# Kernel optimization log

Hardware: AMD Instinct MI355X
Metric: run time of the kernel (lower is better)

Reference implementation:

```python
import jax, jax.numpy as jnp
import numpy as np

MAX_SEQ_LEN = 1000

def _ln(x, g, b, eps=1e-5):
    m = jnp.mean(x, -1, keepdims=True)
    v = jnp.var(x, -1, keepdims=True)
    return (x - m) * jax.lax.rsqrt(v + eps) * g + b

def _conv1d(x, k, b):
    # x [B,T,Cin], k [K,Cin,Cout], 'SAME' padding (odd kernel)
    return jax.lax.conv_general_dilated(x, k, (1,), 'SAME', dimension_numbers=('NWC', 'WIO', 'NWC')) + b

def _dwconv(x, w):
    # lightweight conv: softmax-normalized depthwise kernel, w [C,K]
    k = jnp.transpose(jax.nn.softmax(w, axis=1))[:, None, :]  # [K,1,C]
    return jax.lax.conv_general_dilated(x, k, (1,), 'SAME', dimension_numbers=('NWC', 'WIO', 'NWC'), feature_group_count=x.shape[-1])

def _conv2d(x, k, b):
    # x [B,H,W,Cin], k [kh,kw,Cin,Cout]
    return jax.lax.conv_general_dilated(x, k, (1, 1), 'SAME', dimension_numbers=('NHWC', 'HWIO', 'NHWC')) + b

def _lconv(x, mask, ln_g, ln_b, glu_w, glu_b, dw, out_w, out_b):
    # LConvBlock: LN -> GLU projection -> depthwise lightweight conv -> out proj -> residual, masked
    res = x
    h = _ln(x, ln_g, ln_b)
    h = h @ glu_w + glu_b
    a, g = jnp.split(h, 2, axis=-1)
    h = a * jax.nn.sigmoid(g)
    h = jnp.where(mask[..., None], 0.0, h)
    h = _dwconv(h, dw)
    h = h @ out_w + out_b
    h = h + res
    return jnp.where(mask[..., None], 0.0, h)

def _forward(content_embedding, speaker_embedding_B, rhythm_B, scaled_duration_outputs,
             in_w, in_b,
             lc0_ln_g, lc0_ln_b, lc0_glu_w, lc0_glu_b, lc0_dw, lc0_out_w, lc0_out_b,
             lc1_ln_g, lc1_ln_b, lc1_glu_w, lc1_glu_b, lc1_dw, lc1_out_w, lc1_out_b,
             p1_w, p1_b, p2_k, p2_b,
             cw_k, cw_b, cw_ln_g, cw_ln_b,
             mkb1_k, mkb1_b, mkb2_k, mkb2_b,
             lw_w, lw_b, ln_g, ln_b, text_mask):
    B, S, _ = content_embedding.shape
    spk = jnp.broadcast_to(speaker_embedding_B[:, None, :], (B, S, speaker_embedding_B.shape[-1]))
    x = jnp.concatenate([content_embedding, spk], -1) @ in_w + in_b
    # duration predictor
    V = _lconv(x, text_mask, lc0_ln_g, lc0_ln_b, lc0_glu_w, lc0_glu_b, lc0_dw, lc0_out_w, lc0_out_b)
    V = _lconv(V, text_mask, lc1_ln_g, lc1_ln_b, lc1_glu_w, lc1_glu_b, lc1_dw, lc1_out_w, lc1_out_b)
    D = jax.nn.softplus(V @ p1_w + p1_b)[..., 0]
    D = jnp.where(text_mask, 0.0, D)
    T = _conv1d(V, p2_k, p2_b)  # [B,S,upsampled_dim]
    # learnable upsampling
    pred_phoneme_len = scaled_duration_outputs.sum(-1)
    alpha_B = jax.lax.stop_gradient(pred_phoneme_len / rhythm_B) / D.sum(-1)
    sD = alpha_B[:, None] * D
    sV = alpha_B[:, None, None] * V
    sT = alpha_B[:, None, None] * T
    mel_len = jnp.clip(jnp.round(sD.sum(-1)).astype(jnp.int32), 1, MAX_SEQ_LEN)
    mel_mask = jnp.arange(MAX_SEQ_LEN)[None, :] >= mel_len[:, None]  # True = pad
    attn_mask = mel_mask[:, :, None] & text_mask[:, None, :]  # bmm(mel_mask, src_mask^T).bool()
    e_k = jnp.cumsum(sD, axis=1)
    s_k = e_k - sD
    t = jnp.arange(1, MAX_SEQ_LEN + 1, dtype=sD.dtype)[None, :, None]
    Sm = jnp.where(attn_mask, 0.0, t - s_k[:, None, :])
    Em = jnp.where(attn_mask, 0.0, e_k[:, None, :] - t)
    # conv_w block: conv1d -> relu -> LN
    Cv = _ln(jax.nn.relu(_conv1d(sV, cw_k, cw_b)), cw_ln_g, cw_ln_b)  # [B,S,CW]
    feat = jnp.concatenate([Sm[..., None], Em[..., None],
                            jnp.broadcast_to(Cv[:, None, :, :], (B, MAX_SEQ_LEN, S, Cv.shape[-1]))], -1)
    h = jax.nn.silu(_conv2d(feat, mkb1_k, mkb1_b))
    h = jax.nn.silu(_conv2d(h, mkb2_k, mkb2_b))
    Wsc = (h @ lw_w + lw_b)[..., 0]  # [B,mel,S]
    Wsc = jnp.where(attn_mask | text_mask[:, None, :], -jnp.inf, Wsc)
    Wmat = jax.nn.softmax(Wsc, axis=2)
    up = jnp.matmul(Wmat, sT)
    up = _ln(up, ln_g, ln_b)
    up = jnp.where(mel_mask[..., None], 0.0, up)
    return up, Wmat, alpha_B, mel_len, mel_mask

def setup_inputs() -> dict:
    key = jax.random.key(0)
    ks = iter(jax.random.split(key, 64))
    B, S, DC, DS, H, CW, MKB, K = 8, 256, 192, 64, 256, 16, 16, 3
    def w(shape, scale=0.02):
        return jax.random.normal(next(ks), shape, jnp.float32) * scale
    inp = {}
    inp['content_embedding'] = jax.random.normal(next(ks), (B, S, DC), jnp.float32)
    inp['speaker_embedding_B'] = jax.random.normal(next(ks), (B, DS), jnp.float32)
    inp['rhythm_B'] = 0.15 + 0.1 * jax.random.uniform(next(ks), (B,), jnp.float32)
    inp['scaled_duration_outputs'] = jax.random.uniform(next(ks), (B, S), jnp.float32)
    lens = jax.random.randint(next(ks), (B,), 200, S + 1)
    inp['text_mask'] = jnp.arange(S)[None, :] >= lens[:, None]
    inp['in_w'] = w((DC + DS, H)); inp['in_b'] = jnp.zeros((H,), jnp.float32)
    for i in range(2):
        inp[f'lc{i}_ln_g'] = jnp.ones((H,), jnp.float32); inp[f'lc{i}_ln_b'] = jnp.zeros((H,), jnp.float32)
        inp[f'lc{i}_glu_w'] = w((H, 2 * H)); inp[f'lc{i}_glu_b'] = jnp.zeros((2 * H,), jnp.float32)
        inp[f'lc{i}_dw'] = w((H, K), 1.0)
        inp[f'lc{i}_out_w'] = w((H, H)); inp[f'lc{i}_out_b'] = jnp.zeros((H,), jnp.float32)
    inp['p1_w'] = w((H, 1)); inp['p1_b'] = jnp.zeros((1,), jnp.float32)
    inp['p2_k'] = w((K, H, H)); inp['p2_b'] = jnp.zeros((H,), jnp.float32)
    inp['cw_k'] = w((K, H, CW)); inp['cw_b'] = jnp.zeros((CW,), jnp.float32)
    inp['cw_ln_g'] = jnp.ones((CW,), jnp.float32); inp['cw_ln_b'] = jnp.zeros((CW,), jnp.float32)
    inp['mkb1_k'] = w((K, K, CW + 2, MKB)); inp['mkb1_b'] = jnp.zeros((MKB,), jnp.float32)
    inp['mkb2_k'] = w((K, K, MKB, MKB)); inp['mkb2_b'] = jnp.zeros((MKB,), jnp.float32)
    inp['lw_w'] = w((MKB, 1)); inp['lw_b'] = jnp.zeros((1,), jnp.float32)
    inp['ln_g'] = jnp.ones((H,), jnp.float32); inp['ln_b'] = jnp.zeros((H,), jnp.float32)
    return inp

def reference(content_embedding, speaker_embedding_B, rhythm_B, scaled_duration_outputs,
              text_mask,
              in_w, in_b,
              lc0_ln_g, lc0_ln_b, lc0_glu_w, lc0_glu_b, lc0_dw, lc0_out_w, lc0_out_b,
              lc1_ln_g, lc1_ln_b, lc1_glu_w, lc1_glu_b, lc1_dw, lc1_out_w, lc1_out_b,
              p1_w, p1_b, p2_k, p2_b,
              cw_k, cw_b, cw_ln_g, cw_ln_b,
              mkb1_k, mkb1_b, mkb2_k, mkb2_b,
              lw_w, lw_b, ln_g, ln_b):
    return _forward(content_embedding, speaker_embedding_B, rhythm_B, scaled_duration_outputs,
                    in_w, in_b,
                    lc0_ln_g, lc0_ln_b, lc0_glu_w, lc0_glu_b, lc0_dw, lc0_out_w, lc0_out_b,
                    lc1_ln_g, lc1_ln_b, lc1_glu_w, lc1_glu_b, lc1_dw, lc1_out_w, lc1_out_b,
                    p1_w, p1_b, p2_k, p2_b,
                    cw_k, cw_b, cw_ln_g, cw_ln_b,
                    mkb1_k, mkb1_b, mkb2_k, mkb2_b,
                    lw_w, lw_b, ln_g, ln_b, text_mask)
```

## Files before the change

### kernel.cpp

```cpp
#include <hip/hip_runtime.h>
#include <math.h>

#define SS 256
#define HH 256
#define MLEN 1000
#define CWW 16
#define NOC 16
#define RB 24

typedef __attribute__((ext_vector_type(8))) short bfrag;
typedef __attribute__((ext_vector_type(4))) float ffrag;

#define WS_V2     1048576u
#define WS_STT    1835008u
#define WS_WB     2097152u
#define WS_CCV    2424832u
#define WS_SSV    2457600u
#define WS_CCI    2490368u
#define WS_SSI    2523136u
#define WS_CP     2555904u
#define WS_CV     2654208u
#define WS_EK     2686976u
#define WS_SK     2689024u
#define WS_ALPHA  2691072u
#define WS_MELI   2691080u
#define WS_TMASK  2691088u

#define PK_IN     0u
#define PK_GLU0   65536u
#define PK_GLU1   196608u
#define PK_OUT0   327680u
#define PK_OUT1   393216u
#define PK_P2     458752u

#define OUT_UP    0u
#define OUT_W     2048000u
#define OUT_ALPHA 4096000u
#define OUT_MLEN  4096008u
#define OUT_MMASK 4096016u

__device__ __forceinline__ unsigned bf16rne(float x){
  unsigned u=__float_as_uint(x);
  u += 0x7fffu + ((u>>16)&1u);
  return u;
}
__device__ __forceinline__ unsigned short bf16h(float x){ return (unsigned short)(bf16rne(x)>>16); }
__device__ __forceinline__ float bf2f(unsigned short u){ return __uint_as_float(((unsigned)u)<<16); }
__device__ __forceinline__ unsigned frag_idx(int k,int n,int KT){
  return (unsigned)(((((n>>4)*KT+(k>>5))*64 + ((k>>3)&3)*16 + (n&15))<<3) + (k&7));
}

__global__ __launch_bounds__(256) void k_prepmask(const void* __restrict__ traw,
    const float* __restrict__ in_w,
    const float* __restrict__ g0, const float* __restrict__ g1,
    const float* __restrict__ o0, const float* __restrict__ o1,
    const float* __restrict__ p2k, float* __restrict__ ws){
  int tid=threadIdx.x;
  if(blockIdx.x==256){
    __shared__ int s_fu, s_ff, s_nz;
    const unsigned char* mb=(const unsigned char*)traw;
    const unsigned int*  mw=(const unsigned int*)traw;
    if(tid==0){s_fu=0;s_ff=0;s_nz=0;}
    __syncthreads();
    int fu=0,ff=0,nz=0;
    for(int w=tid;w<512;w+=256){
      unsigned int v=mw[w];
      if(v){ nz=1; if(v==0x3F800000u) ff=1; else if(v&0xFFFFFF00u) fu=1; }
    }
    if(fu) atomicOr(&s_fu,1);
    if(ff) atomicOr(&s_ff,1);
    if(nz) atomicOr(&s_nz,1);
    __syncthreads();
    int words = (s_ff || (!s_fu && s_nz));
    for(int i=tid;i<2048;i+=256){
      unsigned int v = words ? mw[i] : (unsigned int)mb[i];
      ws[WS_TMASK+i] = v ? 1.0f : 0.0f;
    }
    return;
  }
  unsigned short* wb=(unsigned short*)(ws+WS_WB);
  int gid=blockIdx.x*256+tid, stride=65536;
  for(int i=gid;i<65536;i+=stride){ int k=i>>8,n=i&255; wb[PK_IN  +frag_idx(k,n,8)]=bf16h(in_w[i]); }
  for(int i=gid;i<131072;i+=stride){ int k=i>>9,n=i&511; wb[PK_GLU0+frag_idx(k,n,8)]=bf16h(g0[i]); }
  for(int i=gid;i<131072;i+=stride){ int k=i>>9,n=i&511; wb[PK_GLU1+frag_idx(k,n,8)]=bf16h(g1[i]); }
  for(int i=gid;i<65536;i+=stride){ int k=i>>8,n=i&255; wb[PK_OUT0+frag_idx(k,n,8)]=bf16h(o0[i]); }
  for(int i=gid;i<65536;i+=stride){ int k=i>>8,n=i&255; wb[PK_OUT1+frag_idx(k,n,8)]=bf16h(o1[i]); }
  for(int i=gid;i<196608;i+=stride){ int k3=i>>16,r=i&65535,k=r>>8,n=r&255;
    wb[PK_P2+(unsigned)k3*65536u+frag_idx(k,n,8)]=bf16h(p2k[i]); }
}

__global__ __launch_bounds__(256) void k_front(
    const float* __restrict__ ce, const float* __restrict__ spk,
    const unsigned short* __restrict__ wb, const float* __restrict__ in_b,
    const float* __restrict__ g0b, const float* __restrict__ ln0g, const float* __restrict__ ln0b,
    const float* __restrict__ dw0, const float* __restrict__ o0b,
    const float* __restrict__ g1b, const float* __restrict__ ln1g, const float* __restrict__ ln1b,
    const float* __restrict__ dw1, const float* __restrict__ o1b,
    const float* __restrict__ tmask, float* __restrict__ V2){
  __shared__ unsigned short Abf[16][264];
  __shared__ unsigned short Hb[8][264];
  __shared__ float Xf[8][264];
  __shared__ float Vf[8][264];
  __shared__ float dws[2][3][256];
  __shared__ float tmL[8];
  int b=blockIdx.x>>6, tile=blockIdx.x&63, s0=tile*4, tid=threadIdx.x;
  int w=tid>>6, lane=tid&63, lq=lane>>4, lm=lane&15;
  {
    float d0=dw0[tid*3],d1=dw0[tid*3+1],d2=dw0[tid*3+2];
    float mx=fmaxf(d0,fmaxf(d1,d2));
    float e0=__expf(d0-mx),e1=__expf(d1-mx),e2=__expf(d2-mx);
    float inv=1.0f/(e0+e1+e2);
    dws[0][0][tid]=e0*inv; dws[0][1][tid]=e1*inv; dws[0][2][tid]=e2*inv;
    d0=dw1[tid*3];d1=dw1[tid*3+1];d2=dw1[tid*3+2];
    mx=fmaxf(d0,fmaxf(d1,d2));
    e0=__expf(d0-mx);e1=__expf(d1-mx);e2=__expf(d2-mx);
    inv=1.0f/(e0+e1+e2);
    dws[1][0][tid]=e0*inv; dws[1][1][tid]=e1*inv; dws[1][2][tid]=e2*inv;
  }
  if(tid<8){
    int sI=s0-2+tid;
    tmL[tid]=(sI>=0&&sI<256)? tmask[b*256+sI] : 1.0f;
  }
  for(int it=0;it<8;it++){
    float v=0.f;
    int sI=s0-2+it;
    if(sI>=0 && sI<256){
      int m=b*256+sI;
      v=(tid<192)? ce[m*192+tid] : spk[b*64+tid-192];
    }
    Abf[it][tid]=bf16h(v);
  }
  for(int it=8;it<16;it++) Abf[it][tid]=0;
  __syncthreads();
  {
    ffrag acc[4];
    #pragma unroll
    for(int j=0;j<4;j++){acc[j][0]=0;acc[j][1]=0;acc[j][2]=0;acc[j][3]=0;}
    #pragma unroll
    for(int kt=0;kt<8;kt++){
      bfrag af=*(const bfrag*)&Abf[lm][kt*32+lq*8];
      #pragma unroll
      for(int j=0;j<4;j++){
        int nt=w*4+j;
        bfrag bf=*(const bfrag*)(wb+PK_IN+((((unsigned)(nt*8+kt))*64u+(unsigned)lane)<<3));
        acc[j]=__builtin_amdgcn_mfma_f32_16x16x32_bf16(af,bf,acc[j],0,0,0);
      }
    }
    #pragma unroll
    for(int j=0;j<4;j++){
      int n=w*64+j*16+lm;
      float bn=in_b[n];
      #pragma unroll
      for(int reg=0;reg<4;reg++){
        int row=lq*4+reg;
        if(row<8) Xf[row][n]=acc[j][reg]+bn;
      }
    }
  }
  __syncthreads();
  {
    int r=tid>>4, seg=tid&15;
    if(r<8){
      float s=0.f,q=0.f;
      #pragma unroll
      for(int j4=0;j4<4;j4++){
        float4 v=*(const float4*)&Xf[r][seg*16+j4*4];
        s+=v.x+v.y+v.z+v.w; q+=v.x*v.x+v.y*v.y+v.z*v.z+v.w*v.w;
      }
      s+=__shfl_xor(s,1); q+=__shfl_xor(q,1);
      s+=__shfl_xor(s,2); q+=__shfl_xor(q,2);
      s+=__shfl_xor(s,4); q+=__shfl_xor(q,4);
      s+=__shfl_xor(s,8); q+=__shfl_xor(q,8);
      float mean=s*(1.0f/256.0f), rstd=rsqrtf(q*(1.0f/256.0f)-mean*mean+1e-5f);
      #pragma unroll
      for(int j4=0;j4<4;j4++){
        int c=seg*16+j4*4;
        float4 v=*(const float4*)&Xf[r][c];
        unsigned short q0=bf16h((v.x-mean)*rstd*ln0g[c+0]+ln0b[c+0]);
        unsigned short q1=bf16h((v.y-mean)*rstd*ln0g[c+1]+ln0b[c+1]);
        unsigned short q2=bf16h((v.z-mean)*rstd*ln0g[c+2]+ln0b[c+2]);
        unsigned short q3=bf16h((v.w-mean)*rstd*ln0g[c+3]+ln0b[c+3]);
        *(uint2*)&Abf[r][c]=make_uint2((unsigned)q0|((unsigned)q1<<16),(unsigned)q2|((unsigned)q3<<16));
      }
    }
  }
  __syncthreads();
  {
    ffrag aa[4],ag[4];
    #pragma unroll
    for(int j=0;j<4;j++){aa[j][0]=0;aa[j][1]=0;aa[j][2]=0;aa[j][3]=0;
                         ag[j][0]=0;ag[j][1]=0;ag[j][2]=0;ag[j][3]=0;}
    #pragma unroll
    for(int kt=0;kt<8;kt++){
      bfrag af=*(const bfrag*)&Abf[lm][kt*32+lq*8];
      #pragma unroll
      for(int j=0;j<4;j++){
        int nta=w*4+j, ntg=nta+16;
        bfrag bfa=*(const bfrag*)(wb+PK_GLU0+((((unsigned)(nta*8+kt))*64u+(unsigned)lane)<<3));
        bfrag bfg=*(const bfrag*)(wb+PK_GLU0+((((unsigned)(ntg*8+kt))*64u+(unsigned)lane)<<3));
        aa[j]=__builtin_amdgcn_mfma_f32_16x16x32_bf16(af,bfa,aa[j],0,0,0);
        ag[j]=__builtin_amdgcn_mfma_f32_16x16x32_bf16(af,bfg,ag[j],0,0,0);
      }
    }
    __syncthreads();
    #pragma unroll
    for(int j=0;j<4;j++){
      int n=w*64+j*16+lm;
      float ba=g0b[n], bg=g0b[n+256];
      #pragma unroll
      for(int reg=0;reg<4;reg++){
        int row=lq*4+reg;
        if(row<8){
          float a=aa[j][reg]+ba, g=ag[j][reg]+bg;
          float hv=a*(1.0f/(1.0f+__expf(-g)));
          if(tmL[row]!=0.0f) hv=0.0f;
          Hb[row][n]=bf16h(hv);
        }
      }
    }
  }
  __syncthreads();
  {
    float w0=dws[0][0][tid],w1=dws[0][1][tid],w2=dws[0][2][tid];
    for(int r=0;r<6;r++){
      float a=w0*bf2f(Hb[r][tid])+w1*bf2f(Hb[r+1][tid])+w2*bf2f(Hb[r+2][tid]);
      Abf[r][tid]=bf16h(a);
    }
    Abf[6][tid]=0; Abf[7][tid]=0;
  }
  __syncthreads();
  {
    ffrag acc[4];
    #pragma unroll
    for(int j=0;j<4;j++){acc[j][0]=0;acc[j][1]=0;acc[j][2]=0;acc[j][3]=0;}
    #pragma unroll
    for(int kt=0;kt<8;kt++){
      bfrag af=*(const bfrag*)&Abf[lm][kt*32+lq*8];
      #pragma unroll
      for(int j=0;j<4;j++){
        int nt=w*4+j;
        bfrag bf=*(const bfrag*)(wb+PK_OUT0+((((unsigned)(nt*8+kt))*64u+(unsigned)lane)<<3));
        acc[j]=__builtin_amdgcn_mfma_f32_16x16x32_bf16(af,bf,acc[j],0,0,0);
      }
    }
    #pragma unroll
    for(int j=0;j<4;j++){
      int n=w*64+j*16+lm;
      float bn=o0b[n];
      #pragma unroll
      for(int reg=0;reg<4;reg++){
        int row=lq*4+reg;
        if(row<6){
          float v=(tmL[row+1]==0.0f)? acc[j][reg]+bn+Xf[row+1][n] : 0.0f;
          Vf[row][n]=v;
        }
      }
    }
  }
  __syncthreads();
  {
    int r=tid>>4, seg=tid&15;
    if(r<6){
      float s=0.f,q=0.f;
      #pragma unroll
      for(int j4=0;j4<4;j4++){
        float4 v=*(const float4*)&Vf[r][seg*16+j4*4];
        s+=v.x+v.y+v.z+v.w; q+=v.x*v.x+v.y*v.y+v.z*v.z+v.w*v.w;
      }
      s+=__shfl_xor(s,1); q+=__shfl_xor(q,1);
      s+=__shfl_xor(s,2); q+=__shfl_xor(q,2);
      s+=__shfl_xor(s,4); q+=__shfl_xor(q,4);
      s+=__shfl_xor(s,8); q+=__shfl_xor(q,8);
      float mean=s*(1.0f/256.0f), rstd=rsqrtf(q*(1.0f/256.0f)-mean*mean+1e-5f);
      #pragma unroll
      for(int j4=0;j4<4;j4++){
        int c=seg*16+j4*4;
        float4 v=*(const float4*)&Vf[r][c];
        unsigned short q0=bf16h((v.x-mean)*rstd*ln1g[c+0]+ln1b[c+0]);
        unsigned short q1=bf16h((v.y-mean)*rstd*ln1g[c+1]+ln1b[c+1]);
        unsigned short q2=bf16h((v.z-mean)*rstd*ln1g[c+2]+ln1b[c+2]);
        unsigned short q3=bf16h((v.w-mean)*rstd*ln1g[c+3]+ln1b[c+3]);
        *(uint2*)&Abf[r][c]=make_uint2((unsigned)q0|((unsigned)q1<<16),(unsigned)q2|((unsigned)q3<<16));
      }
    }
  }
  __syncthreads();
  {
    ffrag aa[4],ag[4];
    #pragma unroll
    for(int j=0;j<4;j++){aa[j][0]=0;aa[j][1]=0;aa[j][2]=0;aa[j][3]=0;
                         ag[j][0]=0;ag[j][1]=0;ag[j][2]=0;ag[j][3]=0;}
    #pragma unroll
    for(int kt=0;kt<8;kt++){
      bfrag af=*(const bfrag*)&Abf[lm][kt*32+lq*8];
      #pragma unroll
      for(int j=0;j<4;j++){
        int nta=w*4+j, ntg=nta+16;
        bfrag bfa=*(const bfrag*)(wb+PK_GLU1+((((unsigned)(nta*8+kt))*64u+(unsigned)lane)<<3));
        bfrag bfg=*(const bfrag*)(wb+PK_GLU1+((((unsigned)(ntg*8+kt))*64u+(unsigned)lane)<<3));
        aa[j]=__builtin_amdgcn_mfma_f32_16x16x32_bf16(af,bfa,aa[j],0,0,0);
        ag[j]=__builtin_amdgcn_mfma_f32_16x16x32_bf16(af,bfg,ag[j],0,0,0);
      }
    }
    __syncthreads();
    #pragma unroll
    for(int j=0;j<4;j++){
      int n=w*64+j*16+lm;
      float ba=g1b[n], bg=g1b[n+256];
      #pragma unroll
      for(int reg=0;reg<4;reg++){
        int row=lq*4+reg;
        if(row<6){
          float a=aa[j][reg]+ba, g=ag[j][reg]+bg;
          float hv=a*(1.0f/(1.0f+__expf(-g)));
          if(tmL[row+1]!=0.0f) hv=0.0f;
          Hb[row][n]=bf16h(hv);
        }
      }
    }
  }
  __syncthreads();
  {
    float w0=dws[1][0][tid],w1=dws[1][1][tid],w2=dws[1][2][tid];
    for(int r=0;r<4;r++){
      float a=w0*bf2f(Hb[r][tid])+w1*bf2f(Hb[r+1][tid])+w2*bf2f(Hb[r+2][tid]);
      Abf[r][tid]=bf16h(a);
    }
    Abf[4][tid]=0; Abf[5][tid]=0;
  }
  __syncthreads();
  {
    ffrag acc[4];
    #pragma unroll
    for(int j=0;j<4;j++){acc[j][0]=0;acc[j][1]=0;acc[j][2]=0;acc[j][3]=0;}
    #pragma unroll
    for(int kt=0;kt<8;kt++){
      bfrag af=*(const bfrag*)&Abf[lm][kt*32+lq*8];
      #pragma unroll
      for(int j=0;j<4;j++){
        int nt=w*4+j;
        bfrag bf=*(const bfrag*)(wb+PK_OUT1+((((unsigned)(nt*8+kt))*64u+(unsigned)lane)<<3));
        acc[j]=__builtin_amdgcn_mfma_f32_16x16x32_bf16(af,bf,acc[j],0,0,0);
      }
    }
    #pragma unroll
    for(int j=0;j<4;j++){
      int n=w*64+j*16+lm;
      float bn=o1b[n];
      #pragma unroll
      for(int reg=0;reg<4;reg++){
        int row=lq*4+reg;
        if(row<4){
          float v=(tmL[row+2]!=0.0f)? 0.0f : acc[j][reg]+bn+Vf[row+1][n];
          V2[(unsigned)(b*256+s0+row)*256u+n]=v;
        }
      }
    }
  }
}

__global__ __launch_bounds__(256) void k_postdur(const float* __restrict__ V2,
    const unsigned short* __restrict__ wbp2, const float* __restrict__ p2b,
    const float* __restrict__ cwk,
    const float* __restrict__ p1w, const float* __restrict__ p1b,
    const float* __restrict__ sdo, const float* __restrict__ rhythm,
    float* __restrict__ ws, float* __restrict__ outp){
  int bx=blockIdx.x, tid=threadIdx.x;
  if(bx<256){
    __shared__ unsigned short Abf[18][264];
    int m0=(bx>>1)*16, nh=bx&1, b=m0>>8, s0=m0&255;
    for(int it=0;it<18;it++){
      int sI=s0-1+it;
      float v=(sI>=0&&sI<256)? V2[(unsigned)(b*256+sI)*256u+tid] : 0.0f;
      Abf[it][tid]=bf16h(v);
    }
    __syncthreads();
    int w=tid>>6, lane=tid&63, lq=lane>>4, lm=lane&15;
    ffrag acc[2];
    #pragma unroll
    for(int tt=0;tt<2;tt++){ acc[tt][0]=0;acc[tt][1]=0;acc[tt][2]=0;acc[tt][3]=0; }
    for(int k3=0;k3<3;k3++){
      const unsigned short* wb3=wbp2+(unsigned)k3*65536u;
      #pragma unroll
      for(int kt=0;kt<8;kt++){
        bfrag af=*(const bfrag*)&Abf[lm+k3][kt*32+lq*8];
        #pragma unroll
        for(int tt=0;tt<2;tt++){
          int nt=nh*8+w*2+tt;
          bfrag bf=*(const bfrag*)(wb3+((((unsigned)(nt*8+kt))*64u+(unsigned)lane)<<3));
          acc[tt]=__builtin_amdgcn_mfma_f32_16x16x32_bf16(af,bf,acc[tt],0,0,0);
        }
      }
    }
    unsigned short* stt=(unsigned short*)(ws+WS_STT);
    #pragma unroll
    for(int tt=0;tt<2;tt++){
      int n=nh*128+w*32+tt*16+lm;
      float bn=p2b[n];
      unsigned short o0=bf16h(acc[tt][0]+bn);
      unsigned short o1=bf16h(acc[tt][1]+bn);
      unsigned short o2=bf16h(acc[tt][2]+bn);
      unsigned short o3=bf16h(acc[tt][3]+bn);
      *(uint2*)&stt[((unsigned)(b*256+n)<<8)+(unsigned)(s0+lq*4)]=
        make_uint2((unsigned)o0|((unsigned)o1<<16),(unsigned)o2|((unsigned)o3<<16));
    }
  } else if(bx<384){
    __shared__ float Vt[18][SS];
    int bb=bx-256;
    int b=bb>>4, tile=bb&15;
    int sbase=tile*16;
    for(int rr=0;rr<18;rr++){
      int s=sbase-1+rr;
      Vt[rr][tid]=(s>=0&&s<SS)?V2[(b*SS+s)*HH+tid]:0.0f;
    }
    __syncthreads();
    int sl=tid>>4, oc=tid&15;
    float a0=0.f,a1=0.f,a2=0.f,a3=0.f;
    for(int k3=0;k3<3;k3++){
      const float* vp=&Vt[sl+k3][0];
      const float* wpp=cwk+(unsigned)k3*HH*CWW+oc;
      for(int c=0;c<HH;c+=4){
        a0+=vp[c+0]*wpp[(c+0)*CWW];
        a1+=vp[c+1]*wpp[(c+1)*CWW];
        a2+=vp[c+2]*wpp[(c+2)*CWW];
        a3+=vp[c+3]*wpp[(c+3)*CWW];
      }
    }
    ws[WS_CV+(unsigned)(b*SS+sbase+sl)*CWW+oc]=(a0+a1)+(a2+a3);
  } else {
    __shared__ float p1[HH];
    __shared__ float sd[SS];
    __shared__ float red[16];
    int b=bx-384;
    int wid=tid>>6, lane=tid&63;
    p1[tid]=p1w[tid];
    __syncthreads();
    float accd=p1b[0];
    const float* row=V2+(unsigned)(b*SS+tid)*HH;
    for(int k=0;k<HH;k+=4){
      float4 v=*(const float4*)&row[k];
      accd+=v.x*p1[k]+v.y*p1[k+1]+v.z*p1[k+2]+v.w*p1[k+3];
    }
    float Dv=fmaxf(accd,0.0f)+log1pf(expf(-fabsf(accd)));
    if(ws[WS_TMASK+b*SS+tid]!=0.0f) Dv=0.0f;
    float sv=sdo[b*SS+tid];
    float a=Dv, c=sv;
    for(int off=32;off;off>>=1){ a+=__shfl_down(a,off); c+=__shfl_down(c,off); }
    if(lane==0){ red[wid]=a; red[wid+8]=c; }
    __syncthreads();
    float Dsum=red[0]+red[1]+red[2]+red[3];
    float pred=red[8]+red[9]+red[10]+red[11];
    float al=(pred/rhythm[b])/Dsum;
    float sDv=al*Dv;
    sd[tid]=sDv;
    __syncthreads();
    for(int off=1;off<SS;off<<=1){
      float t=(tid>=off)?sd[tid-off]:0.0f;
      __syncthreads();
      sd[tid]+=t;
      __syncthreads();
    }
    float ek=sd[tid], sk=ek-sDv;
    ws[WS_EK+b*SS+tid]=ek;
    ws[WS_SK+b*SS+tid]=sk;
    float melf=sd[SS-1];
    int mel=(int)rintf(melf); mel=mel<1?1:(mel>MLEN?MLEN:mel);
    if(tid==0){
      ws[WS_ALPHA+b]=al;
      ((int*)ws)[WS_MELI+b]=mel;
      outp[OUT_ALPHA+b]=al;
      outp[OUT_MLEN+b]=(float)mel;
    }
    for(int t=tid;t<MLEN;t+=SS) outp[OUT_MMASK+b*MLEN+t]=(t>=mel)?1.0f:0.0f;
  }
}

__global__ __launch_bounds__(256) void k_cp(const float* __restrict__ mkb1k, const float* __restrict__ mkb1b,
    const float* __restrict__ cwb, const float* __restrict__ cwg, const float* __restrict__ cwbe,
    float* __restrict__ ws){
  __shared__ float CvL[258][17];
  __shared__ float k1c[3][3][CWW][NOC];
  __shared__ float kab[3][3][2][NOC];
  __shared__ float skE[258], ekE[258], fiE[258];
  int b=blockIdx.x, tid=threadIdx.x;
  float al=ws[WS_ALPHA+b];
  for(int i=tid;i<3*3*CWW*NOC;i+=256){
    int oc=i&15, ic=(i>>4)&15, kk=i>>8;
    int kw=kk%3, kh=kk/3;
    k1c[kh][kw][ic][oc]=mkb1k[((kh*3+kw)*18+2+ic)*NOC+oc];
  }
  for(int i=tid;i<3*3*2*NOC;i+=256){
    int oc=i&15, ch=(i>>4)&1, kk=i>>5;
    int kw=kk%3, kh=kk/3;
    kab[kh][kw][ch][oc]=mkb1k[((kh*3+kw)*18+ch)*NOC+oc];
  }
  {
    float c[16];
    const float* src=ws+WS_CV+(unsigned)(b*SS+tid)*16u;
    float sm=0.f,qm=0.f;
    #pragma unroll
    for(int ic=0;ic<16;ic++){
      float v=fmaxf(al*src[ic]+cwb[ic],0.0f);
      c[ic]=v; sm+=v; qm+=v*v;
    }
    float mean=sm*(1.0f/16.0f), var=qm*(1.0f/16.0f)-mean*mean;
    float rstd=rsqrtf(var+1e-5f);
    #pragma unroll
    for(int ic=0;ic<16;ic++) CvL[1+tid][ic]=(c[ic]-mean)*rstd*cwg[ic]+cwbe[ic];
  }
  if(tid<CWW){ CvL[0][tid]=0.f; CvL[257][tid]=0.f; }
  if(tid<258){
    float sk=0.f, ek=0.f, fi=0.f;
    if(tid>=1 && tid<=SS){
      sk=ws[WS_SK+b*SS+tid-1];
      ek=ws[WS_EK+b*SS+tid-1];
      fi=(ws[WS_TMASK+b*SS+tid-1]!=0.0f)?0.0f:1.0f;
    }
    skE[tid]=sk; ekE[tid]=ek; fiE[tid]=fi;
  }
  __syncthreads();
  float* cpg=ws+WS_CP+(unsigned)b*3*SS*NOC;
  float ccv[16],ssv[16],cci[16],ssi[16];
  #pragma unroll
  for(int oc=0;oc<NOC;oc++){ float bb2=mkb1b[oc]; ccv[oc]=bb2; cci[oc]=bb2; ssv[oc]=0.f; ssi[oc]=0.f; }
  for(int dt=0;dt<3;dt++){
    float acc[NOC];
    #pragma unroll
    for(int oc=0;oc<NOC;oc++) acc[oc]=0.f;
    #pragma unroll
    for(int ds=0;ds<3;ds++){
      #pragma unroll
      for(int ic=0;ic<CWW;ic++){
        float v=CvL[tid+ds][ic];
        #pragma unroll
        for(int oc=0;oc<NOC;oc++) acc[oc]+=v*k1c[dt][ds][ic][oc];
      }
    }
    for(int oc=0;oc<NOC;oc++) cpg[(unsigned)(dt*SS+tid)*NOC+oc]=acc[oc];
    float va[16],vb[16],ia[16],ib2[16];
    #pragma unroll
    for(int oc=0;oc<NOC;oc++){ va[oc]=0.f; vb[oc]=0.f; ia[oc]=0.f; ib2[oc]=0.f; }
    #pragma unroll
    for(int ds=0;ds<3;ds++){
      int j=tid+ds;
      float inb=(j>=1&&j<=SS)?1.0f:0.0f;
      float fb=fiE[j];
      float skv=skE[j], ekv=ekE[j];
      #pragma unroll
      for(int oc=0;oc<NOC;oc++){
        float ka=kab[dt][ds][0][oc], kb=kab[dt][ds][1][oc];
        float d=ka-kb, e=kb*ekv-ka*skv;
        va[oc]+=inb*d; vb[oc]+=inb*e; ia[oc]+=fb*d; ib2[oc]+=fb*e;
      }
    }
    float dtf=(float)dt;
    #pragma unroll
    for(int oc=0;oc<NOC;oc++){
      ccv[oc]+=acc[oc]+vb[oc]+dtf*va[oc]; ssv[oc]+=va[oc];
      cci[oc]+=acc[oc]+ib2[oc]+dtf*ia[oc]; ssi[oc]+=ia[oc];
    }
  }
  unsigned base=(unsigned)(b*SS+tid)*16u;
  for(int oc=0;oc<NOC;oc++){
    ws[WS_CCV+base+oc]=ccv[oc];
    ws[WS_SSV+base+oc]=ssv[oc];
    ws[WS_CCI+base+oc]=cci[oc];
    ws[WS_SSI+base+oc]=ssi[oc];
  }
}

__global__ __launch_bounds__(256,4) void k_stageB(
    const float* __restrict__ ws, const float* __restrict__ mkb1k, const float* __restrict__ mkb1b,
    const float* __restrict__ mkb2k, const float* __restrict__ mkb2b,
    const float* __restrict__ lww, const float* __restrict__ lwb,
    const float* __restrict__ lng, const float* __restrict__ lnb,
    float* __restrict__ outp){
  __shared__ __align__(16) char smem[3*258*RB*2];
  __shared__ float skL[258], ekL[258];
  __shared__ unsigned char finC[260];
  __shared__ __align__(16) float wscL[SS];
  __shared__ float red[16];
  int bx=blockIdx.x, b=bx/125, chunk=bx%125, t0=chunk*8, tid=threadIdx.x;
  int wid=tid>>6, lane=tid&63;
  int lq=lane>>4, lm=lane&15;
  if(tid<258){
    float sk=0.f, ek=0.f; unsigned char fin=0;
    if(tid>=1 && tid<=SS){
      sk=ws[WS_SK+b*SS+tid-1];
      ek=ws[WS_EK+b*SS+tid-1];
      fin=(ws[WS_TMASK+b*SS+tid-1]!=0.0f)?0:1;
    }
    skL[tid]=sk; ekL[tid]=ek; finC[tid]=fin;
  }
  if(tid<72){
    int sl=tid/24, rem=tid%24;
    int row=(rem<12)?0:257, c=(rem%12)*2;
    *(int*)(smem+((sl*258+row)*RB+c)*2)=0;
  }
  int mel=((const int*)ws)[WS_MELI+b];
  __syncthreads();

  const float* cpb=ws+WS_CP+(unsigned)b*3*SS*NOC;

  unsigned offA[5]; int dtL[5], zgL[5];
  bfrag bfw[5];
  {
    #pragma unroll
    for(int i=0;i<5;i++){
      int g=4*i+lq;
      int dt,ds,hf,zg;
      if(g<18){ dt=g/6; int rm=g-6*dt; ds=rm>>1; hf=rm&1; zg=0; }
      else { dt=0; ds=0; hf=0; zg=1; }
      int srow=wid*64+lm+ds;
      offA[i]=(unsigned)((srow*RB+8*hf)*2);
      dtL[i]=dt; zgL[i]=zg;
      int pk[4];
      if(!zg){
        #pragma unroll
        for(int j=0;j<4;j++){
          unsigned u0=bf16rne(mkb2k[(8*g+2*j)*NOC+lm]);
          unsigned u1=bf16rne(mkb2k[(8*g+2*j+1)*NOC+lm]);
          pk[j]=(int)((u0>>16)|(u1&0xffff0000u));
        }
      } else pk[0]=pk[1]=pk[2]=pk[3]=0;
      bfw[i]=__builtin_bit_cast(bfrag, make_int4(pk[0],pk[1],pk[2],pk[3]));
    }
  }
  float b2v=mkb2b[lm];
  float lwwv=lww[lm];
  float lwb0=lwb[0];
  bfrag azero={};

  auto conv1row=[&](int T){
    int s=tid;
    float acc[NOC];
    bool fv=(T>=1)&&(T<=998)&&(T+1<mel);
    bool fi=(T>=2)&&(T<=998)&&(T-1>=mel);
    if(fv||fi){
      const float* cc=ws+(fv?WS_CCV:WS_CCI)+(unsigned)(b*SS+s)*16u;
      const float* s2=ws+(fv?WS_SSV:WS_SSI)+(unsigned)(b*SS+s)*16u;
      float Tf=(float)T;
      #pragma unroll
      for(int q=0;q<4;q++){
        float4 c4=((const float4*)cc)[q];
        float4 s4=((const float4*)s2)[q];
        acc[4*q+0]=c4.x+Tf*s4.x; acc[4*q+1]=c4.y+Tf*s4.y;
        acc[4*q+2]=c4.z+Tf*s4.z; acc[4*q+3]=c4.w+Tf*s4.w;
      }
    } else {
      #pragma unroll
      for(int oc=0;oc<NOC;oc++) acc[oc]=mkb1b[oc];
      #pragma unroll
      for(int dt=0;dt<3;dt++){
        int tr=T+dt-1;
        if(tr<0||tr>=MLEN) continue;
        bool valid=(tr<mel);
        float tt=(float)(tr+1);
        float gg[3], hh[3];
        #pragma unroll
        for(int ds=0;ds<3;ds++){
          int j=s+ds;
          float f = valid ? ((j>=1&&j<=SS)?1.0f:0.0f) : (float)finC[j];
          gg[ds]=f*(tt-skL[j]);
          hh[ds]=f*(ekL[j]-tt);
        }
        const float* cpr=cpb+(unsigned)(dt*SS+s)*NOC;
        float4 c0=((const float4*)cpr)[0], c1=((const float4*)cpr)[1];
        float4 c2=((const float4*)cpr)[2], c3=((const float4*)cpr)[3];
        acc[0]+=c0.x; acc[1]+=c0.y; acc[2]+=c0.z; acc[3]+=c0.w;
        acc[4]+=c1.x; acc[5]+=c1.y; acc[6]+=c1.z; acc[7]+=c1.w;
        acc[8]+=c2.x; acc[9]+=c2.y; acc[10]+=c2.z; acc[11]+=c2.w;
        acc[12]+=c3.x; acc[13]+=c3.y; acc[14]+=c3.z; acc[15]+=c3.w;
        #pragma unroll
        for(int ds=0;ds<3;ds++){
          const float* kA=mkb1k+((dt*3+ds)*18+0)*NOC;
          const float* kB=mkb1k+((dt*3+ds)*18+1)*NOC;
          #pragma unroll
          for(int oc=0;oc<NOC;oc++) acc[oc]+=gg[ds]*kA[oc]+hh[ds]*kB[oc];
        }
      }
    }
    int slot=T%3;
    int pk[8];
    #pragma unroll
    for(int j=0;j<8;j++){
      float x0=acc[2*j], x1=acc[2*j+1];
      float s0=x0/(1.0f+__expf(-x0));
      float s1=x1/(1.0f+__expf(-x1));
      unsigned u0=bf16rne(s0), u1=bf16rne(s1);
      pk[j]=(int)((u0>>16)|(u1&0xffff0000u));
    }
    int4* dst=(int4*)(smem+((unsigned)(slot*258+s+1)*RB)*2u);
    dst[0]=make_int4(pk[0],pk[1],pk[2],pk[3]);
    dst[1]=make_int4(pk[4],pk[5],pk[6],pk[7]);
  };

  if(t0>0) conv1row(t0-1);
  conv1row(t0);

  #pragma unroll 1
  for(int r=0;r<8;r++){
    int t=t0+r;
    if(t+1<MLEN) conv1row(t+1);
    __syncthreads();
    int tmod=t%3;
    ffrag acc2[4];
    #pragma unroll
    for(int tt=0;tt<4;tt++){ acc2[tt][0]=b2v; acc2[tt][1]=b2v; acc2[tt][2]=b2v; acc2[tt][3]=b2v; }
    #pragma unroll
    for(int i=0;i<5;i++){
      int dt=dtL[i];
      int x=tmod+dt+2; x=(x>=3)?x-3:x; x=(x>=3)?x-3:x;
      int tr=t+dt-1;
      bool av=((unsigned)tr<(unsigned)MLEN)&&(!zgL[i]);
      const char* rp=smem+(unsigned)x*(258u*RB*2u)+offA[i];
      #pragma unroll
      for(int tt=0;tt<4;tt++){
        int4 ra=*(const int4*)(rp+tt*(16*RB*2));
        bfrag a=av?__builtin_bit_cast(bfrag,ra):azero;
        acc2[tt]=__builtin_amdgcn_mfma_f32_16x16x32_bf16(a,bfw[i],acc2[tt],0,0,0);
      }
    }
    #pragma unroll
    for(int tt=0;tt<4;tt++){
      float out4[4];
      #pragma unroll
      for(int q=0;q<4;q++){
        float xx=acc2[tt][q];
        float pv=(xx/(1.0f+__expf(-xx)))*lwwv;
        pv+=__shfl_xor(pv,1); pv+=__shfl_xor(pv,2); pv+=__shfl_xor(pv,4); pv+=__shfl_xor(pv,8);
        out4[q]=pv+lwb0;
      }
      if(lm==0){
        *(float4*)&wscL[wid*64+tt*16+lq*4]=make_float4(out4[0],out4[1],out4[2],out4[3]);
      }
    }
    __syncthreads();
    float fm=(float)finC[tid+1];
    float wsc=wscL[tid];
    float val=(fm!=0.0f)?wsc:-3.0e38f;
    float mx=val;
    for(int off=32;off;off>>=1) mx=fmaxf(mx,__shfl_down(mx,off));
    if(lane==0) red[wid]=mx;
    __syncthreads();
    mx=fmaxf(fmaxf(red[0],red[1]),fmaxf(red[2],red[3]));
    float e=(fm!=0.0f)?__expf(wsc-mx):0.0f;
    float sm=e;
    for(int off=32;off;off>>=1) sm+=__shfl_down(sm,off);
    if(lane==0) red[8+wid]=sm;
    __syncthreads();
    sm=red[8]+red[9]+red[10]+red[11];
    outp[OUT_W+(unsigned)(b*MLEN+t)*SS+tid]=e/sm;
  }

  __syncthreads();
  unsigned short* Wb=(unsigned short*)smem;
  float* UpL=(float*)(smem+8448);
  for(int it=0;it<8;it++){
    Wb[it*264+tid]=bf16h(outp[OUT_W+(unsigned)(b*MLEN+t0+it)*SS+tid]);
  }
  for(int it=8;it<16;it++) Wb[it*264+tid]=0;
  __syncthreads();
  const unsigned short* stt=(const unsigned short*)(ws+WS_STT)+(unsigned)b*65536u;
  ffrag uacc[4];
  #pragma unroll
  for(int tt=0;tt<4;tt++){ uacc[tt][0]=0;uacc[tt][1]=0;uacc[tt][2]=0;uacc[tt][3]=0; }
  #pragma unroll
  for(int kt=0;kt<8;kt++){
    bfrag af=*(const bfrag*)&Wb[lm*264+kt*32+lq*8];
    #pragma unroll
    for(int tt=0;tt<4;tt++){
      int n=wid*64+tt*16+lm;
      bfrag bf=*(const bfrag*)(stt+((unsigned)n<<8)+(unsigned)(kt*32+lq*8));
      uacc[tt]=__builtin_amdgcn_mfma_f32_16x16x32_bf16(af,bf,uacc[tt],0,0,0);
    }
  }
  #pragma unroll
  for(int tt=0;tt<4;tt++){
    #pragma unroll
    for(int reg=0;reg<4;reg++){
      int row=lq*4+reg;
      if(row<8) UpL[row*264+wid*64+tt*16+lm]=uacc[tt][reg];
    }
  }
  __syncthreads();
  {
    int r2=tid>>4, seg=tid&15;
    if(r2<8){
      float s=0.f,q=0.f;
      #pragma unroll
      for(int j4=0;j4<4;j4++){
        float4 v=*(const float4*)&UpL[r2*264+seg*16+j4*4];
        s+=v.x+v.y+v.z+v.w; q+=v.x*v.x+v.y*v.y+v.z*v.z+v.w*v.w;
      }
      s+=__shfl_xor(s,1); q+=__shfl_xor(q,1);
      s+=__shfl_xor(s,2); q+=__shfl_xor(q,2);
      s+=__shfl_xor(s,4); q+=__shfl_xor(q,4);
      s+=__shfl_xor(s,8); q+=__shfl_xor(q,8);
      float mean=s*(1.0f/256.0f), rstd=rsqrtf(q*(1.0f/256.0f)-mean*mean+1e-5f);
      int t=t0+r2;
      bool vld=(t<mel);
      #pragma unroll
      for(int j4=0;j4<4;j4++){
        int c=seg*16+j4*4;
        float4 v=*(const float4*)&UpL[r2*264+c];
        float4 o;
        o.x=vld?((v.x-mean)*rstd*lng[c+0]+lnb[c+0]):0.0f;
        o.y=vld?((v.y-mean)*rstd*lng[c+1]+lnb[c+1]):0.0f;
        o.z=vld?((v.z-mean)*rstd*lng[c+2]+lnb[c+2]):0.0f;
        o.w=vld?((v.w-mean)*rstd*lng[c+3]+lnb[c+3]):0.0f;
        *(float4*)&outp[OUT_UP+(unsigned)(b*MLEN+t)*256u+c]=o;
      }
    }
  }
}

extern "C" void kernel_launch(void* const* d_in, const int* in_sizes, int n_in,
                              void* d_out, int out_size, void* d_ws, size_t ws_size,
                              hipStream_t stream){
  const float* ce   =(const float*)d_in[0];
  const float* spk  =(const float*)d_in[1];
  const float* rhy  =(const float*)d_in[2];
  const float* sdo  =(const float*)d_in[3];
  const void*  tmr  =d_in[4];
  const float* in_w =(const float*)d_in[5];
  const float* in_b =(const float*)d_in[6];
  const float* l0lg =(const float*)d_in[7];
  const float* l0lb =(const float*)d_in[8];
  const float* l0gw =(const float*)d_in[9];
  const float* l0gb =(const float*)d_in[10];
  const float* l0dw =(const float*)d_in[11];
  const float* l0ow =(const float*)d_in[12];
  const float* l0ob =(const float*)d_in[13];
  const float* l1lg =(const float*)d_in[14];
  const float* l1lb =(const float*)d_in[15];
  const float* l1gw =(const float*)d_in[16];
  const float* l1gb =(const float*)d_in[17];
  const float* l1dw =(const float*)d_in[18];
  const float* l1ow =(const float*)d_in[19];
  const float* l1ob =(const float*)d_in[20];
  const float* p1w  =(const float*)d_in[21];
  const float* p1b  =(const float*)d_in[22];
  const float* p2k  =(const float*)d_in[23];
  const float* p2b  =(const float*)d_in[24];
  const float* cwk  =(const float*)d_in[25];
  const float* cwb  =(const float*)d_in[26];
  const float* cwg  =(const float*)d_in[27];
  const float* cwbe =(const float*)d_in[28];
  const float* m1k  =(const float*)d_in[29];
  const float* m1b  =(const float*)d_in[30];
  const float* m2k  =(const float*)d_in[31];
  const float* m2b  =(const float*)d_in[32];
  const float* lww  =(const float*)d_in[33];
  const float* lwbp =(const float*)d_in[34];
  const float* lng  =(const float*)d_in[35];
  const float* lnb  =(const float*)d_in[36];
  float* ws=(float*)d_ws;
  float* outp=(float*)d_out;
  const unsigned short* wbb=(const unsigned short*)(ws+WS_WB);

  k_prepmask<<<257,256,0,stream>>>(tmr, in_w, l0gw, l1gw, l0ow, l1ow, p2k, ws);
  k_front   <<<512,256,0,stream>>>(ce, spk, wbb, in_b,
                                   l0gb, l0lg, l0lb, l0dw, l0ob,
                                   l1gb, l1lg, l1lb, l1dw, l1ob,
                                   ws+WS_TMASK, ws+WS_V2);
  k_postdur <<<392,256,0,stream>>>(ws+WS_V2, wbb+PK_P2, p2b, cwk, p1w, p1b, sdo, rhy, ws, outp);
  k_cp      <<<8,256,0,stream>>>(m1k, m1b, cwb, cwg, cwbe, ws);
  k_stageB  <<<1000,256,0,stream>>>(ws, m1k, m1b, m2k, m2b, lww, lwbp, lng, lnb, outp);
}
```

Baseline: 324.3 us.

## Fuse p2 conv and cw conv into front kernel via halo recompute; merge duration into k_cp

The front kernel's halo widens by one row on each side, so each 4-row tile computes V2 for 6 rows and can run the 3-tap p2 conv (MFMA) and the cw conv directly from shared memory. This removes the separate k_postdur launch and the V2 re-read for those convolutions. The duration/alpha/cumsum work moves into the former k_cp kernel, which saves another launch. In exchange the front kernel does extra halo recomputation and runs the small cw conv with poor parallelism, while the 8-block duration stage stays serial.

```diff
diff --git a/kernel.cpp b/kernel.cpp
--- a/kernel.cpp
+++ b/kernel.cpp
@@ -96,13 +96,15 @@
     const float* __restrict__ dw0, const float* __restrict__ o0b,
     const float* __restrict__ g1b, const float* __restrict__ ln1g, const float* __restrict__ ln1b,
     const float* __restrict__ dw1, const float* __restrict__ o1b,
-    const float* __restrict__ tmask, float* __restrict__ V2){
-  __shared__ unsigned short Abf[16][264];
-  __shared__ unsigned short Hb[8][264];
-  __shared__ float Xf[8][264];
+    const float* __restrict__ p2b, const float* __restrict__ cwk,
+    const float* __restrict__ tmask, float* __restrict__ ws){
+  __shared__ unsigned short Abf[18][264];
+  __shared__ unsigned short Hb[10][264];
+  __shared__ float Xf[10][264];
   __shared__ float Vf[8][264];
   __shared__ float dws[2][3][256];
-  __shared__ float tmL[8];
+  __shared__ float tmL[10];
+  float* V2=ws+WS_V2;
   int b=blockIdx.x>>6, tile=blockIdx.x&63, s0=tile*4, tid=threadIdx.x;
   int w=tid>>6, lane=tid&63, lq=lane>>4, lm=lane&15;
   {
@@ -117,20 +119,20 @@
     inv=1.0f/(e0+e1+e2);
     dws[1][0][tid]=e0*inv; dws[1][1][tid]=e1*inv; dws[1][2][tid]=e2*inv;
   }
-  if(tid<8){
-    int sI=s0-2+tid;
+  if(tid<10){
+    int sI=s0-3+tid;
     tmL[tid]=(sI>=0&&sI<256)? tmask[b*256+sI] : 1.0f;
   }
-  for(int it=0;it<8;it++){
+  for(int it=0;it<10;it++){
     float v=0.f;
-    int sI=s0-2+it;
+    int sI=s0-3+it;
     if(sI>=0 && sI<256){
       int m=b*256+sI;
       v=(tid<192)? ce[m*192+tid] : spk[b*64+tid-192];
     }
     Abf[it][tid]=bf16h(v);
   }
-  for(int it=8;it<16;it++) Abf[it][tid]=0;
+  for(int it=10;it<18;it++) Abf[it][tid]=0;
   __syncthreads();
   {
     ffrag acc[4];
@@ -153,14 +155,14 @@
       #pragma unroll
       for(int reg=0;reg<4;reg++){
         int row=lq*4+reg;
-        if(row<8) Xf[row][n]=acc[j][reg]+bn;
+        if(row<10) Xf[row][n]=acc[j][reg]+bn;
       }
     }
   }
   __syncthreads();
   {
     int r=tid>>4, seg=tid&15;
-    if(r<8){
+    if(r<10){
       float s=0.f,q=0.f;
       #pragma unroll
       for(int j4=0;j4<4;j4++){
@@ -210,7 +212,7 @@
       #pragma unroll
       for(int reg=0;reg<4;reg++){
         int row=lq*4+reg;
-        if(row<8){
+        if(row<10){
           float a=aa[j][reg]+ba, g=ag[j][reg]+bg;
           float hv=a*(1.0f/(1.0f+__expf(-g)));
           if(tmL[row]!=0.0f) hv=0.0f;
@@ -222,11 +224,11 @@
   __syncthreads();
   {
     float w0=dws[0][0][tid],w1=dws[0][1][tid],w2=dws[0][2][tid];
-    for(int r=0;r<6;r++){
+    for(int r=0;r<8;r++){
       float a=w0*bf2f(Hb[r][tid])+w1*bf2f(Hb[r+1][tid])+w2*bf2f(Hb[r+2][tid]);
       Abf[r][tid]=bf16h(a);
     }
-    Abf[6][tid]=0; Abf[7][tid]=0;
+    Abf[8][tid]=0; Abf[9][tid]=0;
   }
   __syncthreads();
   {
@@ -250,7 +252,7 @@
       #pragma unroll
       for(int reg=0;reg<4;reg++){
         int row=lq*4+reg;
-        if(row<6){
+        if(row<8){
           float v=(tmL[row+1]==0.0f)? acc[j][reg]+bn+Xf[row+1][n] : 0.0f;
           Vf[row][n]=v;
         }
@@ -260,7 +262,7 @@
   __syncthreads();
   {
     int r=tid>>4, seg=tid&15;
-    if(r<6){
+    if(r<8){
       float s=0.f,q=0.f;
       #pragma unroll
       for(int j4=0;j4<4;j4++){
@@ -310,7 +312,7 @@
       #pragma unroll
       for(int reg=0;reg<4;reg++){
         int row=lq*4+reg;
-        if(row<6){
+        if(row<8){
           float a=aa[j][reg]+ba, g=ag[j][reg]+bg;
           float hv=a*(1.0f/(1.0f+__expf(-g)));
           if(tmL[row+1]!=0.0f) hv=0.0f;
@@ -322,11 +324,11 @@
   __syncthreads();
   {
     float w0=dws[1][0][tid],w1=dws[1][1][tid],w2=dws[1][2][tid];
-    for(int r=0;r<4;r++){
+    for(int r=0;r<6;r++){
       float a=w0*bf2f(Hb[r][tid])+w1*bf2f(Hb[r+1][tid])+w2*bf2f(Hb[r+2][tid]);
       Abf[r][tid]=bf16h(a);
     }
-    Abf[4][tid]=0; Abf[5][tid]=0;
+    Abf[6][tid]=0; Abf[7][tid]=0;
   }
   __syncthreads();
   {
@@ -343,6 +345,7 @@
         acc[j]=__builtin_amdgcn_mfma_f32_16x16x32_bf16(af,bf,acc[j],0,0,0);
       }
     }
+    __syncthreads();
     #pragma unroll
     for(int j=0;j<4;j++){
       int n=w*64+j*16+lm;
@@ -350,140 +353,85 @@
       #pragma unroll
       for(int reg=0;reg<4;reg++){
         int row=lq*4+reg;
-        if(row<4){
+        if(row<6){
           float v=(tmL[row+2]!=0.0f)? 0.0f : acc[j][reg]+bn+Vf[row+1][n];
-          V2[(unsigned)(b*256+s0+row)*256u+n]=v;
-        }
-      }
-    }
-  }
-}
-
-__global__ __launch_bounds__(256) void k_postdur(const float* __restrict__ V2,
-    const unsigned short* __restrict__ wbp2, const float* __restrict__ p2b,
-    const float* __restrict__ cwk,
-    const float* __restrict__ p1w, const float* __restrict__ p1b,
-    const float* __restrict__ sdo, const float* __restrict__ rhythm,
-    float* __restrict__ ws, float* __restrict__ outp){
-  int bx=blockIdx.x, tid=threadIdx.x;
-  if(bx<256){
-    __shared__ unsigned short Abf[18][264];
-    int m0=(bx>>1)*16, nh=bx&1, b=m0>>8, s0=m0&255;
-    for(int it=0;it<18;it++){
-      int sI=s0-1+it;
-      float v=(sI>=0&&sI<256)? V2[(unsigned)(b*256+sI)*256u+tid] : 0.0f;
-      Abf[it][tid]=bf16h(v);
-    }
-    __syncthreads();
-    int w=tid>>6, lane=tid&63, lq=lane>>4, lm=lane&15;
-    ffrag acc[2];
-    #pragma unroll
-    for(int tt=0;tt<2;tt++){ acc[tt][0]=0;acc[tt][1]=0;acc[tt][2]=0;acc[tt][3]=0; }
+          if(row>=1&&row<=4) V2[(unsigned)(b*256+s0-1+row)*256u+n]=v;
+          Xf[row][n]=v;
+          Abf[row][n]=(unsigned short)(bf16rne(v)>>16);
+        }
+      }
+    }
+  }
+  __syncthreads();
+  {
+    ffrag tacc[4];
+    #pragma unroll
+    for(int tt=0;tt<4;tt++){tacc[tt][0]=0;tacc[tt][1]=0;tacc[tt][2]=0;tacc[tt][3]=0;}
     for(int k3=0;k3<3;k3++){
-      const unsigned short* wb3=wbp2+(unsigned)k3*65536u;
+      const unsigned short* wb3=wb+PK_P2+(unsigned)k3*65536u;
       #pragma unroll
       for(int kt=0;kt<8;kt++){
         bfrag af=*(const bfrag*)&Abf[lm+k3][kt*32+lq*8];
         #pragma unroll
-        for(int tt=0;tt<2;tt++){
-          int nt=nh*8+w*2+tt;
+        for(int tt=0;tt<4;tt++){
+          int nt=w*4+tt;
           bfrag bf=*(const bfrag*)(wb3+((((unsigned)(nt*8+kt))*64u+(unsigned)lane)<<3));
-          acc[tt]=__builtin_amdgcn_mfma_f32_16x16x32_bf16(af,bf,acc[tt],0,0,0);
+          tacc[tt]=__builtin_amdgcn_mfma_f32_16x16x32_bf16(af,bf,tacc[tt],0,0,0);
         }
       }
     }
     unsigned short* stt=(unsigned short*)(ws+WS_STT);
-    #pragma unroll
-    for(int tt=0;tt<2;tt++){
-      int n=nh*128+w*32+tt*16+lm;
-      float bn=p2b[n];
-      unsigned short o0=bf16h(acc[tt][0]+bn);
-      unsigned short o1=bf16h(acc[tt][1]+bn);
-      unsigned short o2=bf16h(acc[tt][2]+bn);
-      unsigned short o3=bf16h(acc[tt][3]+bn);
-      *(uint2*)&stt[((unsigned)(b*256+n)<<8)+(unsigned)(s0+lq*4)]=
-        make_uint2((unsigned)o0|((unsigned)o1<<16),(unsigned)o2|((unsigned)o3<<16));
-    }
-  } else if(bx<384){
-    __shared__ float Vt[18][SS];
-    int bb=bx-256;
-    int b=bb>>4, tile=bb&15;
-    int sbase=tile*16;
-    for(int rr=0;rr<18;rr++){
-      int s=sbase-1+rr;
-      Vt[rr][tid]=(s>=0&&s<SS)?V2[(b*SS+s)*HH+tid]:0.0f;
-    }
-    __syncthreads();
-    int sl=tid>>4, oc=tid&15;
-    float a0=0.f,a1=0.f,a2=0.f,a3=0.f;
-    for(int k3=0;k3<3;k3++){
-      const float* vp=&Vt[sl+k3][0];
-      const float* wpp=cwk+(unsigned)k3*HH*CWW+oc;
-      for(int c=0;c<HH;c+=4){
-        a0+=vp[c+0]*wpp[(c+0)*CWW];
-        a1+=vp[c+1]*wpp[(c+1)*CWW];
-        a2+=vp[c+2]*wpp[(c+2)*CWW];
-        a3+=vp[c+3]*wpp[(c+3)*CWW];
-      }
-    }
-    ws[WS_CV+(unsigned)(b*SS+sbase+sl)*CWW+oc]=(a0+a1)+(a2+a3);
-  } else {
-    __shared__ float p1[HH];
-    __shared__ float sd[SS];
-    __shared__ float red[16];
-    int b=bx-384;
-    int wid=tid>>6, lane=tid&63;
-    p1[tid]=p1w[tid];
-    __syncthreads();
-    float accd=p1b[0];
-    const float* row=V2+(unsigned)(b*SS+tid)*HH;
-    for(int k=0;k<HH;k+=4){
-      float4 v=*(const float4*)&row[k];
-      accd+=v.x*p1[k]+v.y*p1[k+1]+v.z*p1[k+2]+v.w*p1[k+3];
-    }
-    float Dv=fmaxf(accd,0.0f)+log1pf(expf(-fabsf(accd)));
-    if(ws[WS_TMASK+b*SS+tid]!=0.0f) Dv=0.0f;
-    float sv=sdo[b*SS+tid];
-    float a=Dv, c=sv;
-    for(int off=32;off;off>>=1){ a+=__shfl_down(a,off); c+=__shfl_down(c,off); }
-    if(lane==0){ red[wid]=a; red[wid+8]=c; }
-    __syncthreads();
-    float Dsum=red[0]+red[1]+red[2]+red[3];
-    float pred=red[8]+red[9]+red[10]+red[11];
-    float al=(pred/rhythm[b])/Dsum;
-    float sDv=al*Dv;
-    sd[tid]=sDv;
-    __syncthreads();
-    for(int off=1;off<SS;off<<=1){
-      float t=(tid>=off)?sd[tid-off]:0.0f;
+    if(lq==0){
+      #pragma unroll
+      for(int tt=0;tt<4;tt++){
+        int n=(w*4+tt)*16+lm;
+        float bn=p2b[n];
+        #pragma unroll
+        for(int reg=0;reg<4;reg++){
+          int s=s0+reg;
+          stt[(unsigned)(b*256+n)*256u+(unsigned)s]=bf16h(tacc[tt][reg]+bn);
+        }
+      }
+    }
+    {
+      int seg=tid>>6, row=(tid>>4)&3, oc=tid&15;
+      float part=0.f;
+      #pragma unroll
+      for(int k3=0;k3<3;k3++){
+        const float* vp=&Xf[row+k3][seg*64];
+        const float* wp=cwk+(unsigned)k3*HH*CWW+(unsigned)(seg*64)*CWW+oc;
+        for(int c=0;c<64;c+=4){
+          part+=vp[c+0]*wp[(c+0)*CWW]+vp[c+1]*wp[(c+1)*CWW]
+               +vp[c+2]*wp[(c+2)*CWW]+vp[c+3]*wp[(c+3)*CWW];
+        }
+      }
+      float* pr=(float*)Hb;
+      pr[(row*16+oc)*4+seg]=part;
       __syncthreads();
-      sd[tid]+=t;
-      __syncthreads();
-    }
-    float ek=sd[tid], sk=ek-sDv;
-    ws[WS_EK+b*SS+tid]=ek;
-    ws[WS_SK+b*SS+tid]=sk;
-    float melf=sd[SS-1];
-    int mel=(int)rintf(melf); mel=mel<1?1:(mel>MLEN?MLEN:mel);
-    if(tid==0){
-      ws[WS_ALPHA+b]=al;
-      ((int*)ws)[WS_MELI+b]=mel;
-      outp[OUT_ALPHA+b]=al;
-      outp[OUT_MLEN+b]=(float)mel;
-    }
-    for(int t=tid;t<MLEN;t+=SS) outp[OUT_MMASK+b*MLEN+t]=(t>=mel)?1.0f:0.0f;
+      if(tid<64){
+        int r2=tid>>4, oc2=tid&15;
+        float* p4=&pr[tid*4];
+        ws[WS_CV+(unsigned)(b*256+s0+r2)*16u+oc2]=(p4[0]+p4[1])+(p4[2]+p4[3]);
+      }
+    }
   }
 }
 
-__global__ __launch_bounds__(256) void k_cp(const float* __restrict__ mkb1k, const float* __restrict__ mkb1b,
+__global__ __launch_bounds__(256) void k_durcp(const float* __restrict__ V2, const float* __restrict__ p1w,
+    const float* __restrict__ p1b, const float* __restrict__ sdo, const float* __restrict__ rhythm,
+    const float* __restrict__ mkb1k, const float* __restrict__ mkb1b,
     const float* __restrict__ cwb, const float* __restrict__ cwg, const float* __restrict__ cwbe,
-    float* __restrict__ ws){
+    float* __restrict__ ws, float* __restrict__ outp){
   __shared__ float CvL[258][17];
   __shared__ float k1c[3][3][CWW][NOC];
   __shared__ float kab[3][3][2][NOC];
   __shared__ float skE[258], ekE[258], fiE[258];
+  __shared__ float p1[HH];
+  __shared__ float sd[SS];
+  __shared__ float red[16];
   int b=blockIdx.x, tid=threadIdx.x;
-  float al=ws[WS_ALPHA+b];
+  int wid=tid>>6, lane=tid&63;
+  p1[tid]=p1w[tid];
   for(int i=tid;i<3*3*CWW*NOC;i+=256){
     int oc=i&15, ic=(i>>4)&15, kk=i>>8;
     int kw=kk%3, kh=kk/3;
@@ -494,30 +442,63 @@
     int kw=kk%3, kh=kk/3;
     kab[kh][kw][ch][oc]=mkb1k[((kh*3+kw)*18+ch)*NOC+oc];
   }
-  {
-    float c[16];
+  __syncthreads();
+  float accd=p1b[0];
+  const float* row=V2+(unsigned)(b*SS+tid)*HH;
+  for(int k=0;k<HH;k+=4){
+    float4 v=*(const float4*)&row[k];
+    accd+=v.x*p1[k]+v.y*p1[k+1]+v.z*p1[k+2]+v.w*p1[k+3];
+  }
+  float Dv=fmaxf(accd,0.0f)+log1pf(expf(-fabsf(accd)));
+  float tm=ws[WS_TMASK+b*SS+tid];
+  if(tm!=0.0f) Dv=0.0f;
+  float sv=sdo[b*SS+tid];
+  float a=Dv, c=sv;
+  for(int off=32;off;off>>=1){ a+=__shfl_down(a,off); c+=__shfl_down(c,off); }
+  if(lane==0){ red[wid]=a; red[wid+8]=c; }
+  __syncthreads();
+  float Dsum=red[0]+red[1]+red[2]+red[3];
+  float pred=red[8]+red[9]+red[10]+red[11];
+  float al=(pred/rhythm[b])/Dsum;
+  float sDv=al*Dv;
+  sd[tid]=sDv;
+  __syncthreads();
+  for(int off=1;off<SS;off<<=1){
+    float t=(tid>=off)?sd[tid-off]:0.0f;
+    __syncthreads();
+    sd[tid]+=t;
+    __syncthreads();
+  }
+  float ek=sd[tid], sk=ek-sDv;
+  ws[WS_EK+b*SS+tid]=ek;
+  ws[WS_SK+b*SS+tid]=sk;
+  skE[tid+1]=sk; ekE[tid+1]=ek; fiE[tid+1]=(tm!=0.0f)?0.0f:1.0f;
+  float melf=sd[SS-1];
+  int mel=(int)rintf(melf); mel=mel<1?1:(mel>MLEN?MLEN:mel);
+  if(tid==0){
+    ws[WS_ALPHA+b]=al;
+    ((int*)ws)[WS_MELI+b]=mel;
+    outp[OUT_ALPHA+b]=al;
+    outp[OUT_MLEN+b]=(float)mel;
+    skE[0]=0.f; ekE[0]=0.f; fiE[0]=0.f;
+    skE[257]=0.f; ekE[257]=0.f; fiE[257]=0.f;
+  }
+  for(int t=tid;t<MLEN;t+=SS) outp[OUT_MMASK+b*MLEN+t]=(t>=mel)?1.0f:0.0f;
+  {
+    float cc[16];
     const float* src=ws+WS_CV+(unsigned)(b*SS+tid)*16u;
     float sm=0.f,qm=0.f;
     #pragma unroll
     for(int ic=0;ic<16;ic++){
       float v=fmaxf(al*src[ic]+cwb[ic],0.0f);
-      c[ic]=v; sm+=v; qm+=v*v;
+      cc[ic]=v; sm+=v; qm+=v*v;
     }
     float mean=sm*(1.0f/16.0f), var=qm*(1.0f/16.0f)-mean*mean;
     float rstd=rsqrtf(var+1e-5f);
     #pragma unroll
-    for(int ic=0;ic<16;ic++) CvL[1+tid][ic]=(c[ic]-mean)*rstd*cwg[ic]+cwbe[ic];
+    for(int ic=0;ic<16;ic++) CvL[1+tid][ic]=(cc[ic]-mean)*rstd*cwg[ic]+cwbe[ic];
   }
   if(tid<CWW){ CvL[0][tid]=0.f; CvL[257][tid]=0.f; }
-  if(tid<258){
-    float sk=0.f, ek=0.f, fi=0.f;
-    if(tid>=1 && tid<=SS){
-      sk=ws[WS_SK+b*SS+tid-1];
-      ek=ws[WS_EK+b*SS+tid-1];
-      fi=(ws[WS_TMASK+b*SS+tid-1]!=0.0f)?0.0f:1.0f;
-    }
-    skE[tid]=sk; ekE[tid]=ek; fiE[tid]=fi;
-  }
   __syncthreads();
   float* cpg=ws+WS_CP+(unsigned)b*3*SS*NOC;
   float ccv[16],ssv[16],cci[16],ssi[16];
@@ -863,8 +844,7 @@
   k_front   <<<512,256,0,stream>>>(ce, spk, wbb, in_b,
                                    l0gb, l0lg, l0lb, l0dw, l0ob,
                                    l1gb, l1lg, l1lb, l1dw, l1ob,
-                                   ws+WS_TMASK, ws+WS_V2);
-  k_postdur <<<392,256,0,stream>>>(ws+WS_V2, wbb+PK_P2, p2b, cwk, p1w, p1b, sdo, rhy, ws, outp);
-  k_cp      <<<8,256,0,stream>>>(m1k, m1b, cwb, cwg, cwbe, ws);
+                                   p2b, cwk, ws+WS_TMASK, ws);
+  k_durcp   <<<8,256,0,stream>>>(ws+WS_V2, p1w, p1b, sdo, rhy, m1k, m1b, cwb, cwg, cwbe, ws, outp);
   k_stageB  <<<1000,256,0,stream>>>(ws, m1k, m1b, m2k, m2b, lww, lwbp, lng, lnb, outp);
 }
```

Result: slower. 340.8 us (+5.1%).
